# Kernel tuning notes

Hardware: AMD Instinct MI355X
Metric: run time of the kernel (lower is better)

Reference implementation:

```python
import jax, jax.numpy as jnp
import numpy as np

NUM_EXPERTS = 64
TOP_K = 2
AUX_LOSS_COEF = 0.01
Z_LOSS_COEF = 0.001


def setup_inputs() -> dict:
    key = jax.random.key(0)
    k1, k2 = jax.random.split(key)
    hidden_states = jax.random.normal(k1, (4, 4096, 4096), dtype=jnp.float32)
    # nn.Linear(hidden_size, num_experts, bias=False) -> weight [E, H]
    gate_w = jax.random.normal(k2, (NUM_EXPERTS, 4096), dtype=jnp.float32) * 0.02
    return {"hidden_states": hidden_states, "gate_w": gate_w}


def reference(hidden_states, gate_w):
    b, s, h = hidden_states.shape
    # gate projection: [b, s, E]
    router_logits = jnp.einsum("bsh,eh->bse", hidden_states, gate_w)
    # softmax in fp32 as in the torch module
    probs = jax.nn.softmax(router_logits.astype(jnp.float32), axis=-1)
    routing_weights, selected_experts = jax.lax.top_k(probs, TOP_K)
    routing_weights = routing_weights / jnp.sum(routing_weights, axis=-1, keepdims=True)
    routing_weights = routing_weights.astype(hidden_states.dtype)

    # auxiliary load-balancing loss
    num_tokens = b * s
    # scatter_(-1, selected, 1): top-k indices are distinct, so one_hot-sum == set-to-1
    expert_mask = jax.nn.one_hot(selected_experts, NUM_EXPERTS, dtype=router_logits.dtype).sum(axis=-2)  # [b,s,E]
    tokens_per_expert = expert_mask.sum(axis=(0, 1)) / num_tokens          # [E]
    router_prob_per_expert = probs.sum(axis=(0, 1)) / num_tokens           # [E]
    aux_loss = NUM_EXPERTS * jnp.sum(tokens_per_expert * router_prob_per_expert)

    # z-loss: mean of squared logsumexp over experts
    z_loss = jnp.mean(jax.scipy.special.logsumexp(router_logits, axis=-1) ** 2)

    router_loss = AUX_LOSS_COEF * aux_loss + Z_LOSS_COEF * z_loss
    return routing_weights, selected_experts, router_loss
```

## Files before the change

kernel.cpp:

```cpp
#include <hip/hip_runtime.h>
#include <math.h>

#define HDIM 4096
#define NEXP 64
#define NTOK 16384
#define MBLK 32
#define KC   64
#define NCHUNK (HDIM / KC)
#define ASTR 68
#define CSTRIDE 68

typedef float v4f __attribute__((ext_vector_type(4)));

template <int CTRL, int RMASK>
__device__ __forceinline__ float dpp_add(float x) {
    int xi = __builtin_bit_cast(int, x);
    int yi = __builtin_amdgcn_update_dpp(0, xi, CTRL, RMASK, 0xF, true);
    return x + __builtin_bit_cast(float, yi);
}

__device__ __forceinline__ void barrier_lgkm_only() {
    asm volatile("s_waitcnt lgkmcnt(0)\n\ts_barrier" ::: "memory");
}

__global__ __launch_bounds__(512, 2) void router_main(
    const float* __restrict__ hidden,
    const float* __restrict__ gate,
    float* __restrict__ out_rw,
    float* __restrict__ out_sel,
    float* __restrict__ psum_g,
    float* __restrict__ cnt_g,
    float* __restrict__ zsum_g)
{
    __shared__ float A_lds[2][MBLK * ASTR];
    __shared__ float C_lds[MBLK * CSTRIDE];
    __shared__ float rden[MBLK];
    __shared__ unsigned hist[NEXP];

    const int t = threadIdx.x;
    const int lane = t & 63;
    const int wave = __builtin_amdgcn_readfirstlane(t >> 6);
    const int m0 = blockIdx.x * MBLK;
    const int ksub = lane & 15;
    const int esub = lane >> 4;

    const v4f* __restrict__ A4 = (const v4f*)hidden;
    const v4f* __restrict__ G4 = (const v4f*)gate;

    const int st = t >> 4;
    const int sc = t & 15;
    const size_t arow = (size_t)(m0 + st) * (HDIM / 4);

    const size_t grow0 = (size_t)(8 * wave + esub) * (HDIM / 4);
    const size_t grow1 = (size_t)(8 * wave + 4 + esub) * (HDIM / 4);

    float acc[MBLK][2];
#pragma unroll
    for (int tt = 0; tt < MBLK; ++tt) { acc[tt][0] = 0.f; acc[tt][1] = 0.f; }

    v4f apref = __builtin_nontemporal_load(&A4[arow + sc]);
    *(v4f*)&A_lds[0][st * ASTR + sc * 4] = apref;
    apref = __builtin_nontemporal_load(&A4[arow + 16 + sc]);
    v4f gc0 = G4[grow0 + ksub];
    v4f gc1 = G4[grow1 + ksub];
    __syncthreads();

    for (int it = 0; it < NCHUNK; ++it) {
        const int cur = it & 1;
        const int cn = (it + 1 < NCHUNK) ? (it + 1) : (NCHUNK - 1);
        v4f gn0 = G4[grow0 + cn * 16 + ksub];
        v4f gn1 = G4[grow1 + cn * 16 + ksub];
        if (it + 1 < NCHUNK)
            *(v4f*)&A_lds[cur ^ 1][st * ASTR + sc * 4] = apref;
        const int ca = (it + 2 < NCHUNK) ? (it + 2) : (NCHUNK - 1);
        apref = __builtin_nontemporal_load(&A4[arow + ca * 16 + sc]);
        const float* Ab = &A_lds[cur][ksub * 4];
#pragma unroll
        for (int tt = 0; tt < MBLK; ++tt) {
            v4f a = *(const v4f*)&Ab[tt * ASTR];
            acc[tt][0] = fmaf(a.x, gc0.x, acc[tt][0]);
            acc[tt][0] = fmaf(a.y, gc0.y, acc[tt][0]);
            acc[tt][0] = fmaf(a.z, gc0.z, acc[tt][0]);
            acc[tt][0] = fmaf(a.w, gc0.w, acc[tt][0]);
            acc[tt][1] = fmaf(a.x, gc1.x, acc[tt][1]);
            acc[tt][1] = fmaf(a.y, gc1.y, acc[tt][1]);
            acc[tt][1] = fmaf(a.z, gc1.z, acc[tt][1]);
            acc[tt][1] = fmaf(a.w, gc1.w, acc[tt][1]);
        }
        barrier_lgkm_only();
        gc0 = gn0;
        gc1 = gn1;
    }

#pragma unroll
    for (int tt = 0; tt < MBLK; ++tt)
#pragma unroll
        for (int eg = 0; eg < 2; ++eg) {
            float x = acc[tt][eg];
            x = dpp_add<0xB1,  0xF>(x);
            x = dpp_add<0x4E,  0xF>(x);
            x = dpp_add<0x141, 0xF>(x);
            x = dpp_add<0x140, 0xF>(x);
            acc[tt][eg] = x;
        }
    if (ksub == 0) {
#pragma unroll
        for (int tt = 0; tt < MBLK; ++tt) {
            C_lds[tt * CSTRIDE + wave * 8 + esub]     = acc[tt][0];
            C_lds[tt * CSTRIDE + wave * 8 + 4 + esub] = acc[tt][1];
        }
    }

    if (t < NEXP) hist[t] = 0u;
    __syncthreads();

    if (wave != 0) return;

    float z = 0.f;
    if (lane < MBLK) {
        float v1 = -INFINITY, v2 = -INFINITY;
        int i1 = 0, i2 = 0;
        for (int e = 0; e < NEXP; ++e) {
            float v = C_lds[lane * CSTRIDE + e];
            if (v > v1)      { v2 = v1; i2 = i1; v1 = v; i1 = e; }
            else if (v > v2) { v2 = v;  i2 = e; }
        }
        atomicAdd(&hist[i1], 1u);
        atomicAdd(&hist[i2], 1u);

        float d = 0.f;
        for (int e = 0; e < NEXP; ++e) {
            float ev = expf(C_lds[lane * CSTRIDE + e] - v1);
            C_lds[lane * CSTRIDE + e] = ev;
            d += ev;
        }
        rden[lane] = 1.0f / d;
        float lse = v1 + logf(d);
        z = lse * lse;

        float e2 = expf(v2 - v1);
        float w2 = e2 / (1.f + e2);
        float w1 = 1.f - w2;
        int tok = m0 + lane;
        out_rw[2 * tok + 0] = w1;
        out_rw[2 * tok + 1] = w2;
        out_sel[2 * tok + 0] = (float)i1;
        out_sel[2 * tok + 1] = (float)i2;
    }

#pragma unroll
    for (int off = 32; off > 0; off >>= 1) z += __shfl_down(z, off);
    if (lane == 0) atomicAdd(zsum_g, z);

    float ps = 0.f;
    for (int m = 0; m < MBLK; ++m)
        ps += C_lds[m * CSTRIDE + lane] * rden[m];
    atomicAdd(&psum_g[lane], ps);
    atomicAdd(&cnt_g[lane], (float)hist[lane]);
}

__global__ void router_final(const float* __restrict__ ws, float* __restrict__ out_loss)
{
    int e = threadIdx.x;
    const float inv = 1.0f / (float)NTOK;
    float p = (ws[64 + e] * inv) * (ws[e] * inv);
#pragma unroll
    for (int off = 32; off > 0; off >>= 1) p += __shfl_down(p, off);
    if (e == 0)
        out_loss[0] = 0.01f * (64.f * p) + 0.001f * (ws[128] * inv);
}

extern "C" void kernel_launch(void* const* d_in, const int* in_sizes, int n_in,
                              void* d_out, int out_size, void* d_ws, size_t ws_size,
                              hipStream_t stream) {
    const float* hidden = (const float*)d_in[0];
    const float* gate   = (const float*)d_in[1];
    float* out = (float*)d_out;
    float* ws  = (float*)d_ws;

    hipMemsetAsync(d_ws, 0, 129 * sizeof(float), stream);
    router_main<<<dim3(NTOK / MBLK), dim3(512), 0, stream>>>(
        hidden, gate,
        out,
        out + NTOK * 2,
        ws, ws + 64, ws + 128);
    router_final<<<dim3(1), dim3(64), 0, stream>>>(ws, out + NTOK * 4);
}
```

Measured before the change: 448.2 us.

## Compute router GEMM with bf16x3 split MFMA instead of scalar FP32 FMA

Replaces the scalar FP32 FMA dot-product loop with MFMA 32x32x8 bf16 instructions. Both hidden and gate values are split into three bf16 parts, and six cross-product MFMAs approximate FP32 accuracy. The token tile doubles to 64, and eight waves split the 64x64 output into four quadrants by two K halves, with the halves combined through LDS. It targets the compute-bound FMA inner loop, at the cost of extra conversion work during staging, an occupancy bound of one block per CU, and a small accuracy risk that could change top-k selection on near ties.

New measurement: 429.9 us. 4.1% less time.

```diff
diff --git a/kernel.cpp b/kernel.cpp
--- a/kernel.cpp
+++ b/kernel.cpp
@@ -4,26 +4,48 @@
 #define HDIM 4096
 #define NEXP 64
 #define NTOK 16384
-#define MBLK 32
+#define MBLK 64
 #define KC   64
 #define NCHUNK (HDIM / KC)
-#define ASTR 68
 #define CSTRIDE 68
 
 typedef float v4f __attribute__((ext_vector_type(4)));
-
-template <int CTRL, int RMASK>
-__device__ __forceinline__ float dpp_add(float x) {
-    int xi = __builtin_bit_cast(int, x);
-    int yi = __builtin_amdgcn_update_dpp(0, xi, CTRL, RMASK, 0xF, true);
-    return x + __builtin_bit_cast(float, yi);
+typedef short bh4 __attribute__((ext_vector_type(4)));
+typedef float f32x16 __attribute__((ext_vector_type(16)));
+
+#if defined(__has_builtin)
+#if __has_builtin(__builtin_amdgcn_mfma_f32_32x32x8bf16_1k)
+#define HAVE_MFMA_BUILTIN 1
+#endif
+#endif
+
+__device__ __forceinline__ f32x16 mfma_bf16(bh4 a, bh4 b, f32x16 c) {
+#ifdef HAVE_MFMA_BUILTIN
+    return __builtin_amdgcn_mfma_f32_32x32x8bf16_1k(a, b, c, 0, 0, 0);
+#else
+    asm("v_mfma_f32_32x32x8_bf16 %0, %1, %2, %0" : "+v"(c) : "v"(a), "v"(b));
+    return c;
+#endif
 }
 
 __device__ __forceinline__ void barrier_lgkm_only() {
     asm volatile("s_waitcnt lgkmcnt(0)\n\ts_barrier" ::: "memory");
 }
 
-__global__ __launch_bounds__(512, 2) void router_main(
+__device__ __forceinline__ void split3(float v, unsigned short& h0,
+                                       unsigned short& h1, unsigned short& h2) {
+    unsigned b0 = __builtin_bit_cast(unsigned, v);
+    unsigned r0 = (b0 + 0x7FFFu + ((b0 >> 16) & 1u)) & 0xFFFF0000u;
+    h0 = (unsigned short)(r0 >> 16);
+    float v1 = v - __builtin_bit_cast(float, r0);
+    unsigned b1 = __builtin_bit_cast(unsigned, v1);
+    unsigned r1 = (b1 + 0x7FFFu + ((b1 >> 16) & 1u)) & 0xFFFF0000u;
+    h1 = (unsigned short)(r1 >> 16);
+    float v2 = v1 - __builtin_bit_cast(float, r1);
+    h2 = (unsigned short)(__builtin_bit_cast(unsigned, v2) >> 16);
+}
+
+__global__ __launch_bounds__(512, 1) void router_main(
     const float* __restrict__ hidden,
     const float* __restrict__ gate,
     float* __restrict__ out_rw,
@@ -32,7 +54,8 @@
     float* __restrict__ cnt_g,
     float* __restrict__ zsum_g)
 {
-    __shared__ float A_lds[2][MBLK * ASTR];
+    __shared__ uint2 frag[2][2][3][2][8][64];
+    __shared__ float Pacc[4][16][64];
     __shared__ float C_lds[MBLK * CSTRIDE];
     __shared__ float rden[MBLK];
     __shared__ unsigned hist[NEXP];
@@ -41,83 +64,104 @@
     const int lane = t & 63;
     const int wave = __builtin_amdgcn_readfirstlane(t >> 6);
     const int m0 = blockIdx.x * MBLK;
-    const int ksub = lane & 15;
-    const int esub = lane >> 4;
+    const int c = wave & 3, h = wave >> 2;
+    const int mtp = c & 1, ntp = c >> 1;
 
     const v4f* __restrict__ A4 = (const v4f*)hidden;
     const v4f* __restrict__ G4 = (const v4f*)gate;
 
-    const int st = t >> 4;
-    const int sc = t & 15;
-    const size_t arow = (size_t)(m0 + st) * (HDIM / 4);
-
-    const size_t grow0 = (size_t)(8 * wave + esub) * (HDIM / 4);
-    const size_t grow1 = (size_t)(8 * wave + 4 + esub) * (HDIM / 4);
-
-    float acc[MBLK][2];
-#pragma unroll
-    for (int tt = 0; tt < MBLK; ++tt) { acc[tt][0] = 0.f; acc[tt][1] = 0.f; }
-
-    v4f apref = __builtin_nontemporal_load(&A4[arow + sc]);
-    *(v4f*)&A_lds[0][st * ASTR + sc * 4] = apref;
-    apref = __builtin_nontemporal_load(&A4[arow + 16 + sc]);
-    v4f gc0 = G4[grow0 + ksub];
-    v4f gc1 = G4[grow1 + ksub];
+    const int sr = t >> 3;
+    const int sk = t & 7;
+    const size_t abase = (size_t)(m0 + sr) * (HDIM / 4) + sk * 2;
+    const size_t gbase = (size_t)sr * (HDIM / 4) + sk * 2;
+
+    auto stage = [&](int buf, int ab, v4f x0, v4f x1) {
+        float av[8] = {x0.x, x0.y, x0.z, x0.w, x1.x, x1.y, x1.z, x1.w};
+        unsigned short hs[3][8];
+#pragma unroll
+        for (int u = 0; u < 8; ++u) split3(av[u], hs[0][u], hs[1][u], hs[2][u]);
+        const int half = sr >> 5, rl = sr & 31;
+#pragma unroll
+        for (int p = 0; p < 3; ++p) {
+            frag[buf][ab][p][half][sk][rl ^ (sk << 3)] =
+                make_uint2((unsigned)hs[p][0] | ((unsigned)hs[p][1] << 16),
+                           (unsigned)hs[p][2] | ((unsigned)hs[p][3] << 16));
+            frag[buf][ab][p][half][sk][(32 + rl) ^ (sk << 3)] =
+                make_uint2((unsigned)hs[p][4] | ((unsigned)hs[p][5] << 16),
+                           (unsigned)hs[p][6] | ((unsigned)hs[p][7] << 16));
+        }
+    };
+
+    v4f pa0 = __builtin_nontemporal_load(&A4[abase]);
+    v4f pa1 = __builtin_nontemporal_load(&A4[abase + 1]);
+    v4f pg0 = G4[gbase];
+    v4f pg1 = G4[gbase + 1];
+    stage(0, 0, pa0, pa1);
+    stage(0, 1, pg0, pg1);
+    pa0 = __builtin_nontemporal_load(&A4[abase + 16]);
+    pa1 = __builtin_nontemporal_load(&A4[abase + 17]);
+    pg0 = G4[gbase + 16];
+    pg1 = G4[gbase + 17];
     __syncthreads();
+
+    f32x16 acc{};
 
     for (int it = 0; it < NCHUNK; ++it) {
         const int cur = it & 1;
-        const int cn = (it + 1 < NCHUNK) ? (it + 1) : (NCHUNK - 1);
-        v4f gn0 = G4[grow0 + cn * 16 + ksub];
-        v4f gn1 = G4[grow1 + cn * 16 + ksub];
-        if (it + 1 < NCHUNK)
-            *(v4f*)&A_lds[cur ^ 1][st * ASTR + sc * 4] = apref;
-        const int ca = (it + 2 < NCHUNK) ? (it + 2) : (NCHUNK - 1);
-        apref = __builtin_nontemporal_load(&A4[arow + ca * 16 + sc]);
-        const float* Ab = &A_lds[cur][ksub * 4];
-#pragma unroll
-        for (int tt = 0; tt < MBLK; ++tt) {
-            v4f a = *(const v4f*)&Ab[tt * ASTR];
-            acc[tt][0] = fmaf(a.x, gc0.x, acc[tt][0]);
-            acc[tt][0] = fmaf(a.y, gc0.y, acc[tt][0]);
-            acc[tt][0] = fmaf(a.z, gc0.z, acc[tt][0]);
-            acc[tt][0] = fmaf(a.w, gc0.w, acc[tt][0]);
-            acc[tt][1] = fmaf(a.x, gc1.x, acc[tt][1]);
-            acc[tt][1] = fmaf(a.y, gc1.y, acc[tt][1]);
-            acc[tt][1] = fmaf(a.z, gc1.z, acc[tt][1]);
-            acc[tt][1] = fmaf(a.w, gc1.w, acc[tt][1]);
+        if (it + 1 < NCHUNK) {
+            stage(cur ^ 1, 0, pa0, pa1);
+            stage(cur ^ 1, 1, pg0, pg1);
+        }
+        if (it + 2 < NCHUNK) {
+            const size_t off = (size_t)(it + 2) * 16;
+            pa0 = __builtin_nontemporal_load(&A4[abase + off]);
+            pa1 = __builtin_nontemporal_load(&A4[abase + off + 1]);
+            pg0 = G4[gbase + off];
+            pg1 = G4[gbase + off + 1];
+        }
+#pragma unroll
+        for (int s = 0; s < 4; ++s) {
+            const int k8 = h * 4 + s;
+            const int slot = lane ^ (k8 << 3);
+            bh4 a0 = __builtin_bit_cast(bh4, frag[cur][0][0][mtp][k8][slot]);
+            bh4 a1 = __builtin_bit_cast(bh4, frag[cur][0][1][mtp][k8][slot]);
+            bh4 a2 = __builtin_bit_cast(bh4, frag[cur][0][2][mtp][k8][slot]);
+            bh4 b0 = __builtin_bit_cast(bh4, frag[cur][1][0][ntp][k8][slot]);
+            bh4 b1 = __builtin_bit_cast(bh4, frag[cur][1][1][ntp][k8][slot]);
+            bh4 b2 = __builtin_bit_cast(bh4, frag[cur][1][2][ntp][k8][slot]);
+            acc = mfma_bf16(a0, b0, acc);
+            acc = mfma_bf16(a1, b0, acc);
+            acc = mfma_bf16(a0, b1, acc);
+            acc = mfma_bf16(a1, b1, acc);
+            acc = mfma_bf16(a2, b0, acc);
+            acc = mfma_bf16(a0, b2, acc);
         }
         barrier_lgkm_only();
-        gc0 = gn0;
-        gc1 = gn1;
-    }
-
-#pragma unroll
-    for (int tt = 0; tt < MBLK; ++tt)
-#pragma unroll
-        for (int eg = 0; eg < 2; ++eg) {
-            float x = acc[tt][eg];
-            x = dpp_add<0xB1,  0xF>(x);
-            x = dpp_add<0x4E,  0xF>(x);
-            x = dpp_add<0x141, 0xF>(x);
-            x = dpp_add<0x140, 0xF>(x);
-            acc[tt][eg] = x;
-        }
-    if (ksub == 0) {
-#pragma unroll
-        for (int tt = 0; tt < MBLK; ++tt) {
-            C_lds[tt * CSTRIDE + wave * 8 + esub]     = acc[tt][0];
-            C_lds[tt * CSTRIDE + wave * 8 + 4 + esub] = acc[tt][1];
-        }
-    }
-
+    }
+
+    asm volatile("s_nop 7\n\ts_nop 7\n\ts_nop 7" :::);
+
+    if (h == 1) {
+#pragma unroll
+        for (int r = 0; r < 16; ++r) Pacc[c][r][lane] = acc[r];
+    }
     if (t < NEXP) hist[t] = 0u;
     __syncthreads();
+    if (h == 0) {
+#pragma unroll
+        for (int r = 0; r < 16; ++r) {
+            float x = acc[r] + Pacc[c][r][lane];
+            const int tok = mtp * 32 + (r & 3) + 8 * (r >> 2) + 4 * (lane >> 5);
+            const int e = ntp * 32 + (lane & 31);
+            C_lds[tok * CSTRIDE + e] = x;
+        }
+    }
+    __syncthreads();
 
     if (wave != 0) return;
 
     float z = 0.f;
-    if (lane < MBLK) {
+    {
         float v1 = -INFINITY, v2 = -INFINITY;
         int i1 = 0, i2 = 0;
         for (int e = 0; e < NEXP; ++e) {
```
